# Kernel tuning notes

Hardware: AMD Instinct MI355X
Metric: run time of the kernel (lower is better)

Reference implementation:

```python
import jax, jax.numpy as jnp
import numpy as np

NUM_HEADS = 12
D_MODEL = 768


def setup_inputs() -> dict:
    key = jax.random.key(0)
    k1, k2, k3 = jax.random.split(key, 3)
    proj_std = (2.0 / (D_MODEL + D_MODEL)) ** 0.5
    in_features = jax.random.normal(k1, (4, 2048, D_MODEL), dtype=jnp.float32)
    qkv_proj_weight = (jax.random.truncated_normal(k2, -3.0, 3.0, (3, D_MODEL, D_MODEL), dtype=jnp.float32) * proj_std)
    o_proj_weight = (jax.random.truncated_normal(k3, -3.0, 3.0, (D_MODEL, D_MODEL), dtype=jnp.float32) * proj_std)
    return {"in_features": in_features, "qkv_proj_weight": qkv_proj_weight, "o_proj_weight": o_proj_weight}


def _attention(x, qkv_w, o_w):
    b, s, d = x.shape
    h = NUM_HEADS
    dk = d // h
    # Q,K,V: x @ W^T where W is (out, in) = ((h dk), d_model)
    qkv = jnp.einsum('bsd,tod->tbso', x, qkv_w)  # (3, b, s, d)
    qkv = qkv.reshape(3, b, s, h, dk).transpose(0, 1, 3, 2, 4)  # (3, b, h, s, dk)
    Q, K, V = qkv[0], qkv[1], qkv[2]
    scores = jnp.einsum('bhqd,bhkd->bhqk', Q, K) / jnp.sqrt(jnp.float32(dk))
    causal = jnp.tril(jnp.ones((s, s), dtype=bool))
    scores = jnp.where(causal, scores, -jnp.inf)
    A = jax.nn.softmax(scores, axis=-1)
    O = jnp.einsum('bhqk,bhkd->bhqd', A, V)  # (b, h, s, dk)
    O = O.transpose(0, 2, 1, 3).reshape(b, s, d)
    return jnp.einsum('bsd,od->bso', O, o_w)


def reference(in_features, qkv_proj_weight, o_proj_weight):
    return _attention(in_features, qkv_proj_weight, o_proj_weight)
```

## Files before the change

### kernel.cpp

```cpp
#include <hip/hip_runtime.h>
#include <hip/hip_bf16.h>
#include <stdint.h>

#define SEQ 2048
#define NB 4
#define NH 12
#define DMODEL 768
#define DK 64
#define NTOK (NB*SEQ)
#define QSCALE 0.18033688011f

#define N_X4   (NTOK*DMODEL/4)
#define N_WQ4  (3*DMODEL*DMODEL/4)
#define N_WO4  (DMODEL*DMODEL/4)

typedef __bf16 bf16_t;
typedef __attribute__((ext_vector_type(4))) bf16_t bf16x4;
typedef __attribute__((ext_vector_type(8))) bf16_t bf16x8;
typedef __attribute__((ext_vector_type(4))) float f32x4;

typedef __attribute__((address_space(3))) uint32_t lds_u32_t;
typedef const __attribute__((address_space(1))) uint32_t glb_u32_t;

__device__ inline void load_lds16(const void* g, void* l) {
    __builtin_amdgcn_global_load_lds((glb_u32_t*)g, (lds_u32_t*)l, 16, 0, 0);
}

__global__ void cvt_all(const float* __restrict__ x, const float* __restrict__ wq,
                        const float* __restrict__ wo, bf16_t* __restrict__ dst) {
    int i = blockIdx.x * blockDim.x + threadIdx.x;
    const float* src; int off;
    if (i < N_X4)              { src = x;  off = i; }
    else if (i < N_X4 + N_WQ4) { src = wq; off = i - N_X4; }
    else                       { src = wo; off = i - (N_X4 + N_WQ4); }
    float4 v = ((const float4*)src)[off];
    bf16x4 o;
    o[0] = (bf16_t)v.x; o[1] = (bf16_t)v.y; o[2] = (bf16_t)v.z; o[3] = (bf16_t)v.w;
    ((bf16x4*)dst)[i] = o;
}

#define QSTAGE(AS, BS, KB) do { \
    _Pragma("unroll") \
    for (int j = 0; j < 5; j++) { \
        int c = tid + j*256; \
        if (c < 512) { \
            int row = c >> 2, cb = (c & 3) * 8; \
            load_lds16(Ap_ + (size_t)(mt*128 + row)*DMODEL + (KB) + cb, AS + c*8); \
        } else { \
            int c2 = c - 512; \
            int row = c2 >> 2, cb = (c2 & 3) * 8; \
            load_lds16(Bp_ + (size_t)(nt*192 + row)*DMODEL + (KB) + cb, BS + c2*8); \
        } \
    } \
} while (0)

#define QCOMPUTE(AS, BS) do { \
    bf16x8 af[4]; \
    _Pragma("unroll") \
    for (int f = 0; f < 4; f++) \
        af[f] = *(const bf16x8*)(AS + (wy*64 + f*16 + lr)*32 + lq*8); \
    _Pragma("unroll") \
    for (int fn = 0; fn < 6; fn++) { \
        bf16x8 bfr = *(const bf16x8*)(BS + (wx*96 + fn*16 + lr)*32 + lq*8); \
        _Pragma("unroll") \
        for (int fm = 0; fm < 4; fm++) \
            acc[fm][fn] = __builtin_amdgcn_mfma_f32_16x16x32_bf16(af[fm], bfr, acc[fm][fn], 0, 0, 0); \
    } \
} while (0)

__global__ __launch_bounds__(256, 3) void gemm_qkv(
    const bf16_t* __restrict__ Ap_, const bf16_t* __restrict__ Bp_,
    bf16_t* __restrict__ Qo, bf16_t* __restrict__ Ko, bf16_t* __restrict__ VTo)
{
    __shared__ bf16_t As0[128*32];
    __shared__ bf16_t Bs0[192*32];
    __shared__ bf16_t As1[128*32];
    __shared__ bf16_t Bs1[192*32];
    const int mt = blockIdx.x, nt = blockIdx.y;
    const int tid = threadIdx.x;
    const int w = tid >> 6, lane = tid & 63;
    const int wx = w & 1, wy = w >> 1;
    const int lr = lane & 15, lq = lane >> 4;

    f32x4 acc[4][6] = {};
    QSTAGE(As0, Bs0, 0);
    for (int kb = 0; kb < DMODEL; kb += 64) {
        __syncthreads();
        QSTAGE(As1, Bs1, kb + 32);
        QCOMPUTE(As0, Bs0);
        __syncthreads();
        if (kb + 64 < DMODEL) QSTAGE(As0, Bs0, kb + 64);
        QCOMPUTE(As1, Bs1);
    }

    const int t = nt >> 2;
    const int ob = (nt & 3) * 192 + wx * 96;
    if (t == 2) {
        #pragma unroll
        for (int fm = 0; fm < 4; fm++)
            #pragma unroll
            for (int fn = 0; fn < 6; fn++) {
                int m0 = mt*128 + wy*64 + fm*16 + lq*4;
                int o = ob + fn*16 + lr;
                int b = m0 >> 11, s0 = m0 & 2047;
                int h = o >> 6, dk = o & 63;
                bf16x4 v4;
                #pragma unroll
                for (int r = 0; r < 4; r++) v4[r] = (bf16_t)acc[fm][fn][r];
                *(bf16x4*)(VTo + (size_t)((b*NH + h)*DK + dk)*SEQ + s0) = v4;
            }
    } else {
        #pragma unroll
        for (int fm = 0; fm < 4; fm++)
            #pragma unroll
            for (int fn = 0; fn < 6; fn++)
                #pragma unroll
                for (int r = 0; r < 4; r++) {
                    int m = mt*128 + wy*64 + fm*16 + lq*4 + r;
                    int o = ob + fn*16 + lr;
                    int b = m >> 11, s = m & 2047;
                    int h = o >> 6, dk = o & 63;
                    float v = acc[fm][fn][r];
                    if (t == 0) Qo[(size_t)((b*NH + h)*SEQ + s)*DK + dk] = (bf16_t)(v * QSCALE);
                    else        Ko[(size_t)((b*NH + h)*SEQ + s)*DK + dk] = (bf16_t)v;
                }
    }
}

#define OSTAGE(AS, BS, KB) do { \
    _Pragma("unroll") \
    for (int j = 0; j < 3; j++) { \
        int c = tid + j*256; \
        if (c < 512) { \
            int row = c >> 2, cb = (c & 3) * 8; \
            load_lds16(Ap_ + (size_t)(mt*128 + row)*DMODEL + (KB) + cb, AS + c*8); \
        } else { \
            int c2 = c - 512; \
            int row = c2 >> 2, cb = (c2 & 3) * 8; \
            load_lds16(Bp_ + (size_t)(nt*64 + row)*DMODEL + (KB) + cb, BS + c2*8); \
        } \
    } \
} while (0)

#define OCOMPUTE(AS, BS) do { \
    bf16x8 af[4], bfr[2]; \
    _Pragma("unroll") \
    for (int f = 0; f < 4; f++) \
        af[f]  = *(const bf16x8*)(AS + (wy*64 + f*16 + lr)*32 + lq*8); \
    _Pragma("unroll") \
    for (int f = 0; f < 2; f++) \
        bfr[f] = *(const bf16x8*)(BS + (wx*32 + f*16 + lr)*32 + lq*8); \
    _Pragma("unroll") \
    for (int fm = 0; fm < 4; fm++) \
        _Pragma("unroll") \
        for (int fn = 0; fn < 2; fn++) \
            acc[fm][fn] = __builtin_amdgcn_mfma_f32_16x16x32_bf16(af[fm], bfr[fn], acc[fm][fn], 0, 0, 0); \
} while (0)

__global__ __launch_bounds__(256, 4) void gemm_oproj(
    const bf16_t* __restrict__ Ap_, const bf16_t* __restrict__ Bp_, float* __restrict__ out)
{
    __shared__ bf16_t As0[128*32];
    __shared__ bf16_t Bs0[64*32];
    __shared__ bf16_t As1[128*32];
    __shared__ bf16_t Bs1[64*32];
    const int mt = blockIdx.x, nt = blockIdx.y;
    const int tid = threadIdx.x;
    const int w = tid >> 6, lane = tid & 63;
    const int wx = w & 1, wy = w >> 1;
    const int lr = lane & 15, lq = lane >> 4;

    f32x4 acc[4][2] = {};
    OSTAGE(As0, Bs0, 0);
    for (int kb = 0; kb < DMODEL; kb += 64) {
        __syncthreads();
        OSTAGE(As1, Bs1, kb + 32);
        OCOMPUTE(As0, Bs0);
        __syncthreads();
        if (kb + 64 < DMODEL) OSTAGE(As0, Bs0, kb + 64);
        OCOMPUTE(As1, Bs1);
    }

    #pragma unroll
    for (int fm = 0; fm < 4; fm++)
        #pragma unroll
        for (int fn = 0; fn < 2; fn++)
            #pragma unroll
            for (int r = 0; r < 4; r++) {
                int m = mt*128 + wy*64 + fm*16 + lq*4 + r;
                int n = nt*64 + wx*32 + fn*16 + lr;
                out[(size_t)m*DMODEL + n] = acc[fm][fn][r];
            }
}

#define ASTAGE(KS, VS, KB) do { \
    _Pragma("unroll") \
    for (int j = 0; j < 2; j++) { \
        int rr = w*16 + j*8 + srow; \
        int kperm = (j*8 + srow)*4 + w;   \
        load_lds16(Kp + (size_t)((KB) + kperm)*DK + g*8,  &KS[w*1024 + j*512 + lane*8]); \
        load_lds16(Vp + (size_t)rr*SEQ + (KB) + g*8,   &VS[w*1024 + j*512 + lane*8]); \
    } \
} while (0)

#define STRIP(A0, A1, ACC, AL, MASKED) do { \
    f32x4 sc[4]; \
    _Pragma("unroll") \
    for (int ct = 0; ct < 4; ct++) { \
        f32x4 s = {}; \
        s = __builtin_amdgcn_mfma_f32_16x16x32_bf16(A0, bk[ct][0], s, 0, 0, 0); \
        s = __builtin_amdgcn_mfma_f32_16x16x32_bf16(A1, bk[ct][1], s, 0, 0, 0); \
        sc[ct] = s; \
    } \
    _Pragma("unroll") \
    for (int r = 0; r < 4; r++) { \
        bf16x4 p4; \
        _Pragma("unroll") \
        for (int ct = 0; ct < 4; ct++) { \
            float p = __builtin_amdgcn_exp2f(sc[ct][r]); \
            if (MASKED) { \
                int kl = lr*4 + ct, ql = w*16 + lq*4 + r; \
                p = (kl <= ql) ? p : 0.0f; \
            } \
            p4[ct] = (bf16_t)p; \
        } \
        *(bf16x4*)(Pw + ((((lr>>3)*512 + (lq*4 + r + 16*((lr>>1)&3))*8 + (lr&1)*4)) ^ (((lr>>1)&3) << 4))) = p4; \
    } \
    { \
        bf16x8 ap0 = *(const bf16x8*)(Pw + ((lane ^ (lq<<1))*8)); \
        bf16x8 ap1 = *(const bf16x8*)(Pw + 512 + ((lane ^ (lq<<1))*8)); \
        _Pragma("unroll") \
        for (int c = 0; c < 4; c++) { \
            ACC[c] = __builtin_amdgcn_mfma_f32_16x16x32_bf16(ap0, bv[c][0], ACC[c], 0, 0, 0); \
            ACC[c] = __builtin_amdgcn_mfma_f32_16x16x32_bf16(ap1, bv[c][1], ACC[c], 0, 0, 0); \
        } \
        AL = __builtin_amdgcn_mfma_f32_16x16x32_bf16(ap0, ones, AL, 0, 0, 0); \
        AL = __builtin_amdgcn_mfma_f32_16x16x32_bf16(ap1, ones, AL, 0, 0, 0); \
    } \
} while (0)

#define AITER(KSC, VSC, KSN, VSN, T) do { \
    __syncthreads(); \
    if ((T) + 1 < nIter) ASTAGE(KSN, VSN, ((T)+1)*64); \
    bf16x8 bk[4][2], bv[4][2]; \
    const int sw = lr & 7; \
    _Pragma("unroll") \
    for (int ct = 0; ct < 4; ct++) { \
        int row = ct*16 + lr; \
        bk[ct][0] = *(const bf16x8*)(&KSC[row*64 + ((lq    ) ^ sw)*8]); \
        bk[ct][1] = *(const bf16x8*)(&KSC[row*64 + ((lq + 4) ^ sw)*8]); \
        bv[ct][0] = *(const bf16x8*)(&VSC[row*64 + ((lq    ) ^ sw)*8]); \
        bv[ct][1] = *(const bf16x8*)(&VSC[row*64 + ((lq + 4) ^ sw)*8]); \
    } \
    if ((T) <= qtA) { \
        if ((T) == qtA) { STRIP(aqA0, aqA1, accA, alA, true); } \
        else            { STRIP(aqA0, aqA1, accA, alA, false); } \
    } \
    if ((T) == nIter - 1) { STRIP(aqB0, aqB1, accB, alB, true); } \
    else                  { STRIP(aqB0, aqB1, accB, alB, false); } \
} while (0)

__global__ __launch_bounds__(256, 3) void attn(
    const bf16_t* __restrict__ Q, const bf16_t* __restrict__ K,
    const bf16_t* __restrict__ VT, bf16_t* __restrict__ O)
{
    __shared__ bf16_t Ks0[64*64];
    __shared__ bf16_t Vs0[64*64];
    __shared__ bf16_t Ks1[64*64];
    __shared__ bf16_t Vs1[64*64];
    __shared__ bf16_t P[4][1024];

    const int bh  = blockIdx.x;
    const int qtA = blockIdx.y;
    const int qtB = 31 - qtA;
    const int w = threadIdx.x >> 6, lane = threadIdx.x & 63;
    const int lr = lane & 15, lq = lane >> 4;
    const int qsA = qtA*64 + w*16;
    const int qsB = qtB*64 + w*16;
    const int srow = lane >> 3;
    const int g    = (lane & 7) ^ srow;

    const bf16_t* Qp = Q  + (size_t)bh*SEQ*DK;
    const bf16_t* Kp = K  + (size_t)bh*SEQ*DK;
    const bf16_t* Vp = VT + (size_t)bh*DK*SEQ;
    bf16_t* Pw = &P[w][0];

    const bf16x8 aqA0 = *(const bf16x8*)(Qp + (size_t)(qsA+lr)*DK + lq*8);
    const bf16x8 aqA1 = *(const bf16x8*)(Qp + (size_t)(qsA+lr)*DK + 32 + lq*8);
    const bf16x8 aqB0 = *(const bf16x8*)(Qp + (size_t)(qsB+lr)*DK + lq*8);
    const bf16x8 aqB1 = *(const bf16x8*)(Qp + (size_t)(qsB+lr)*DK + 32 + lq*8);

    bf16x8 ones;
    #pragma unroll
    for (int i = 0; i < 8; i++) ones[i] = (bf16_t)1.0f;

    f32x4 accA[4] = {}, accB[4] = {};
    f32x4 alA = {}, alB = {};

    const int nIter = 32 - qtA;

    ASTAGE(Ks0, Vs0, 0);
    int t = 0;
    while (true) {
        AITER(Ks0, Vs0, Ks1, Vs1, t); t++;
        if (t >= nIter) break;
        AITER(Ks1, Vs1, Ks0, Vs0, t); t++;
        if (t >= nIter) break;
    }

    const int b = bh / NH, h = bh % NH;
    #pragma unroll
    for (int r = 0; r < 4; r++) {
        float rlA = 1.0f / alA[r];
        float rlB = 1.0f / alB[r];
        int qa = qsA + lq*4 + r;
        int qb = qsB + lq*4 + r;
        bf16_t* opA = O + (size_t)(b*SEQ + qa)*DMODEL + h*DK;
        bf16_t* opB = O + (size_t)(b*SEQ + qb)*DMODEL + h*DK;
        #pragma unroll
        for (int c = 0; c < 4; c++) {
            opA[c*16 + lr] = (bf16_t)(accA[c][r] * rlA);
            opB[c*16 + lr] = (bf16_t)(accB[c][r] * rlB);
        }
    }
}

extern "C" void kernel_launch(void* const* d_in, const int* in_sizes, int n_in,
                              void* d_out, int out_size, void* d_ws, size_t ws_size,
                              hipStream_t stream) {
    const float* x    = (const float*)d_in[0];
    const float* wqkv = (const float*)d_in[1];
    const float* wo   = (const float*)d_in[2];
    float* out = (float*)d_out;

    char* ws = (char*)d_ws;
    const size_t SZ_X   = (size_t)NTOK*DMODEL*2;
    const size_t SZ_WQ  = (size_t)3*DMODEL*DMODEL*2;
    const size_t SZ_WO  = (size_t)DMODEL*DMODEL*2;
    const size_t SZ_HD  = (size_t)NB*NH*SEQ*DK*2;
    bf16_t* xb    = (bf16_t*)(ws);
    bf16_t* wqkvb = (bf16_t*)(ws + SZ_X);
    bf16_t* wob   = (bf16_t*)(ws + SZ_X + SZ_WQ);
    bf16_t* Qb    = (bf16_t*)(ws + SZ_X + SZ_WQ + SZ_WO);
    bf16_t* Kb    = (bf16_t*)(ws + SZ_X + SZ_WQ + SZ_WO + SZ_HD);
    bf16_t* VTb   = (bf16_t*)(ws + SZ_X + SZ_WQ + SZ_WO + 2*SZ_HD);
    bf16_t* Ob    = (bf16_t*)(ws + SZ_X + SZ_WQ + SZ_WO + 3*SZ_HD);

    cvt_all<<<(N_X4 + N_WQ4 + N_WO4) / 256, 256, 0, stream>>>(x, wqkv, wo, xb);

    gemm_qkv<<<dim3(NTOK/128, 3*DMODEL/192), 256, 0, stream>>>(xb, wqkvb, Qb, Kb, VTb);
    attn<<<dim3(NB*NH, 16), 256, 0, stream>>>(Qb, Kb, VTb, Ob);
    gemm_oproj<<<dim3(NTOK/128, DMODEL/64), 256, 0, stream>>>(Ob, wob, out);
}
```

Before: 178.9 us.

## Replace paired causal q-tile blocks with one q-tile per block, longest first

Measured after the change: 216.1 us. 1.21x slower.

```diff
diff --git a/kernel.cpp b/kernel.cpp
--- a/kernel.cpp
+++ b/kernel.cpp
@@ -252,15 +252,11 @@
         bv[ct][0] = *(const bf16x8*)(&VSC[row*64 + ((lq    ) ^ sw)*8]); \
         bv[ct][1] = *(const bf16x8*)(&VSC[row*64 + ((lq + 4) ^ sw)*8]); \
     } \
-    if ((T) <= qtA) { \
-        if ((T) == qtA) { STRIP(aqA0, aqA1, accA, alA, true); } \
-        else            { STRIP(aqA0, aqA1, accA, alA, false); } \
-    } \
-    if ((T) == nIter - 1) { STRIP(aqB0, aqB1, accB, alB, true); } \
-    else                  { STRIP(aqB0, aqB1, accB, alB, false); } \
-} while (0)
-
-__global__ __launch_bounds__(256, 3) void attn(
+    if ((T) == nIter - 1) { STRIP(aq0, aq1, acc, al, true); } \
+    else                  { STRIP(aq0, aq1, acc, al, false); } \
+} while (0)
+
+__global__ __launch_bounds__(256, 4) void attn(
     const bf16_t* __restrict__ Q, const bf16_t* __restrict__ K,
     const bf16_t* __restrict__ VT, bf16_t* __restrict__ O)
 {
@@ -271,12 +267,10 @@
     __shared__ bf16_t P[4][1024];
 
     const int bh  = blockIdx.x;
-    const int qtA = blockIdx.y;
-    const int qtB = 31 - qtA;
+    const int qt  = 31 - blockIdx.y;
     const int w = threadIdx.x >> 6, lane = threadIdx.x & 63;
     const int lr = lane & 15, lq = lane >> 4;
-    const int qsA = qtA*64 + w*16;
-    const int qsB = qtB*64 + w*16;
+    const int qs = qt*64 + w*16;
     const int srow = lane >> 3;
     const int g    = (lane & 7) ^ srow;
 
@@ -285,19 +279,17 @@
     const bf16_t* Vp = VT + (size_t)bh*DK*SEQ;
     bf16_t* Pw = &P[w][0];
 
-    const bf16x8 aqA0 = *(const bf16x8*)(Qp + (size_t)(qsA+lr)*DK + lq*8);
-    const bf16x8 aqA1 = *(const bf16x8*)(Qp + (size_t)(qsA+lr)*DK + 32 + lq*8);
-    const bf16x8 aqB0 = *(const bf16x8*)(Qp + (size_t)(qsB+lr)*DK + lq*8);
-    const bf16x8 aqB1 = *(const bf16x8*)(Qp + (size_t)(qsB+lr)*DK + 32 + lq*8);
+    const bf16x8 aq0 = *(const bf16x8*)(Qp + (size_t)(qs+lr)*DK + lq*8);
+    const bf16x8 aq1 = *(const bf16x8*)(Qp + (size_t)(qs+lr)*DK + 32 + lq*8);
 
     bf16x8 ones;
     #pragma unroll
     for (int i = 0; i < 8; i++) ones[i] = (bf16_t)1.0f;
 
-    f32x4 accA[4] = {}, accB[4] = {};
-    f32x4 alA = {}, alB = {};
-
-    const int nIter = 32 - qtA;
+    f32x4 acc[4] = {};
+    f32x4 al = {};
+
+    const int nIter = qt + 1;
 
     ASTAGE(Ks0, Vs0, 0);
     int t = 0;
@@ -311,17 +303,12 @@
     const int b = bh / NH, h = bh % NH;
     #pragma unroll
     for (int r = 0; r < 4; r++) {
-        float rlA = 1.0f / alA[r];
-        float rlB = 1.0f / alB[r];
-        int qa = qsA + lq*4 + r;
-        int qb = qsB + lq*4 + r;
-        bf16_t* opA = O + (size_t)(b*SEQ + qa)*DMODEL + h*DK;
-        bf16_t* opB = O + (size_t)(b*SEQ + qb)*DMODEL + h*DK;
+        float rl = 1.0f / al[r];
+        int q = qs + lq*4 + r;
+        bf16_t* op = O + (size_t)(b*SEQ + q)*DMODEL + h*DK;
         #pragma unroll
-        for (int c = 0; c < 4; c++) {
-            opA[c*16 + lr] = (bf16_t)(accA[c][r] * rlA);
-            opB[c*16 + lr] = (bf16_t)(accB[c][r] * rlB);
-        }
+        for (int c = 0; c < 4; c++)
+            op[c*16 + lr] = (bf16_t)(acc[c][r] * rl);
     }
 }
 
@@ -349,6 +336,6 @@
     cvt_all<<<(N_X4 + N_WQ4 + N_WO4) / 256, 256, 0, stream>>>(x, wqkv, wo, xb);
 
     gemm_qkv<<<dim3(NTOK/128, 3*DMODEL/192), 256, 0, stream>>>(xb, wqkvb, Qb, Kb, VTb);
-    attn<<<dim3(NB*NH, 16), 256, 0, stream>>>(Qb, Kb, VTb, Ob);
+    attn<<<dim3(NB*NH, 32), 256, 0, stream>>>(Qb, Kb, VTb, Ob);
     gemm_oproj<<<dim3(NTOK/128, DMODEL/64), 256, 0, stream>>>(Ob, wob, out);
 }
```

## Keep softmax probabilities in registers via transposed score MFMA, drop LDS round-trip

Applied to the files above, without the earlier changes.

After: 176.3 us. No clear change (-1.4%).

```diff
diff --git a/kernel.cpp b/kernel.cpp
--- a/kernel.cpp
+++ b/kernel.cpp
@@ -197,45 +197,42 @@
     _Pragma("unroll") \
     for (int j = 0; j < 2; j++) { \
         int rr = w*16 + j*8 + srow; \
-        int kperm = (j*8 + srow)*4 + w;   \
+        int kperm = (w>>1)*32 + (j*2 + (srow>>2))*8 + (w&1)*4 + (srow&3);   \
         load_lds16(Kp + (size_t)((KB) + kperm)*DK + g*8,  &KS[w*1024 + j*512 + lane*8]); \
         load_lds16(Vp + (size_t)rr*SEQ + (KB) + g*8,   &VS[w*1024 + j*512 + lane*8]); \
     } \
 } while (0)
 
-#define STRIP(A0, A1, ACC, AL, MASKED) do { \
+#define STRIP(A0, A1, ACC, DL, MASKED) do { \
     f32x4 sc[4]; \
     _Pragma("unroll") \
     for (int ct = 0; ct < 4; ct++) { \
         f32x4 s = {}; \
-        s = __builtin_amdgcn_mfma_f32_16x16x32_bf16(A0, bk[ct][0], s, 0, 0, 0); \
-        s = __builtin_amdgcn_mfma_f32_16x16x32_bf16(A1, bk[ct][1], s, 0, 0, 0); \
+        s = __builtin_amdgcn_mfma_f32_16x16x32_bf16(bk[ct][0], A0, s, 0, 0, 0); \
+        s = __builtin_amdgcn_mfma_f32_16x16x32_bf16(bk[ct][1], A1, s, 0, 0, 0); \
         sc[ct] = s; \
     } \
-    _Pragma("unroll") \
-    for (int r = 0; r < 4; r++) { \
-        bf16x4 p4; \
+    bf16x8 ap0, ap1; \
+    _Pragma("unroll") \
+    for (int ct = 0; ct < 4; ct++) { \
         _Pragma("unroll") \
-        for (int ct = 0; ct < 4; ct++) { \
+        for (int r = 0; r < 4; r++) { \
             float p = __builtin_amdgcn_exp2f(sc[ct][r]); \
             if (MASKED) { \
-                int kl = lr*4 + ct, ql = w*16 + lq*4 + r; \
+                int kl = (ct>>1)*32 + lq*8 + (ct&1)*4 + r; \
+                int ql = w*16 + lr; \
                 p = (kl <= ql) ? p : 0.0f; \
             } \
-            p4[ct] = (bf16_t)p; \
+            bf16_t pb = (bf16_t)p; \
+            DL += (float)pb; \
+            if (ct < 2) ap0[(ct&1)*4 + r] = pb; \
+            else        ap1[(ct&1)*4 + r] = pb; \
         } \
-        *(bf16x4*)(Pw + ((((lr>>3)*512 + (lq*4 + r + 16*((lr>>1)&3))*8 + (lr&1)*4)) ^ (((lr>>1)&3) << 4))) = p4; \
-    } \
-    { \
-        bf16x8 ap0 = *(const bf16x8*)(Pw + ((lane ^ (lq<<1))*8)); \
-        bf16x8 ap1 = *(const bf16x8*)(Pw + 512 + ((lane ^ (lq<<1))*8)); \
-        _Pragma("unroll") \
-        for (int c = 0; c < 4; c++) { \
-            ACC[c] = __builtin_amdgcn_mfma_f32_16x16x32_bf16(ap0, bv[c][0], ACC[c], 0, 0, 0); \
-            ACC[c] = __builtin_amdgcn_mfma_f32_16x16x32_bf16(ap1, bv[c][1], ACC[c], 0, 0, 0); \
-        } \
-        AL = __builtin_amdgcn_mfma_f32_16x16x32_bf16(ap0, ones, AL, 0, 0, 0); \
-        AL = __builtin_amdgcn_mfma_f32_16x16x32_bf16(ap1, ones, AL, 0, 0, 0); \
+    } \
+    _Pragma("unroll") \
+    for (int c = 0; c < 4; c++) { \
+        ACC[c] = __builtin_amdgcn_mfma_f32_16x16x32_bf16(ap0, bv[c][0], ACC[c], 0, 0, 0); \
+        ACC[c] = __builtin_amdgcn_mfma_f32_16x16x32_bf16(ap1, bv[c][1], ACC[c], 0, 0, 0); \
     } \
 } while (0)
 
@@ -253,11 +250,11 @@
         bv[ct][1] = *(const bf16x8*)(&VSC[row*64 + ((lq + 4) ^ sw)*8]); \
     } \
     if ((T) <= qtA) { \
-        if ((T) == qtA) { STRIP(aqA0, aqA1, accA, alA, true); } \
-        else            { STRIP(aqA0, aqA1, accA, alA, false); } \
-    } \
-    if ((T) == nIter - 1) { STRIP(aqB0, aqB1, accB, alB, true); } \
-    else                  { STRIP(aqB0, aqB1, accB, alB, false); } \
+        if ((T) == qtA) { STRIP(aqA0, aqA1, accA, dlA, true); } \
+        else            { STRIP(aqA0, aqA1, accA, dlA, false); } \
+    } \
+    if ((T) == nIter - 1) { STRIP(aqB0, aqB1, accB, dlB, true); } \
+    else                  { STRIP(aqB0, aqB1, accB, dlB, false); } \
 } while (0)
 
 __global__ __launch_bounds__(256, 3) void attn(
@@ -268,7 +265,6 @@
     __shared__ bf16_t Vs0[64*64];
     __shared__ bf16_t Ks1[64*64];
     __shared__ bf16_t Vs1[64*64];
-    __shared__ bf16_t P[4][1024];
 
     const int bh  = blockIdx.x;
     const int qtA = blockIdx.y;
@@ -283,19 +279,14 @@
     const bf16_t* Qp = Q  + (size_t)bh*SEQ*DK;
     const bf16_t* Kp = K  + (size_t)bh*SEQ*DK;
     const bf16_t* Vp = VT + (size_t)bh*DK*SEQ;
-    bf16_t* Pw = &P[w][0];
 
     const bf16x8 aqA0 = *(const bf16x8*)(Qp + (size_t)(qsA+lr)*DK + lq*8);
     const bf16x8 aqA1 = *(const bf16x8*)(Qp + (size_t)(qsA+lr)*DK + 32 + lq*8);
     const bf16x8 aqB0 = *(const bf16x8*)(Qp + (size_t)(qsB+lr)*DK + lq*8);
     const bf16x8 aqB1 = *(const bf16x8*)(Qp + (size_t)(qsB+lr)*DK + 32 + lq*8);
 
-    bf16x8 ones;
-    #pragma unroll
-    for (int i = 0; i < 8; i++) ones[i] = (bf16_t)1.0f;
-
     f32x4 accA[4] = {}, accB[4] = {};
-    f32x4 alA = {}, alB = {};
+    float dlA = 0.0f, dlB = 0.0f;
 
     const int nIter = 32 - qtA;
 
@@ -308,11 +299,14 @@
         if (t >= nIter) break;
     }
 
+    dlA += __shfl_xor(dlA, 16, 64); dlA += __shfl_xor(dlA, 32, 64);
+    dlB += __shfl_xor(dlB, 16, 64); dlB += __shfl_xor(dlB, 32, 64);
+
     const int b = bh / NH, h = bh % NH;
     #pragma unroll
     for (int r = 0; r < 4; r++) {
-        float rlA = 1.0f / alA[r];
-        float rlB = 1.0f / alB[r];
+        float rlA = 1.0f / __shfl(dlA, lq*4 + r, 64);
+        float rlB = 1.0f / __shfl(dlB, lq*4 + r, 64);
         int qa = qsA + lq*4 + r;
         int qb = qsB + lq*4 + r;
         bf16_t* opA = O + (size_t)(b*SEQ + qa)*DMODEL + h*DK;
```

## Keep attention P in registers via transposed QK^T; swizzle GEMM LDS tiles

Applied to the files above, without the earlier changes.

Result: faster. 174.3 us (-2.5%).

```diff
diff --git a/kernel.cpp b/kernel.cpp
--- a/kernel.cpp
+++ b/kernel.cpp
@@ -44,11 +44,11 @@
     for (int j = 0; j < 5; j++) { \
         int c = tid + j*256; \
         if (c < 512) { \
-            int row = c >> 2, cb = (c & 3) * 8; \
+            int row = c >> 2, cb = ((c & 3) ^ ((c >> 3) & 3)) * 8; \
             load_lds16(Ap_ + (size_t)(mt*128 + row)*DMODEL + (KB) + cb, AS + c*8); \
         } else { \
             int c2 = c - 512; \
-            int row = c2 >> 2, cb = (c2 & 3) * 8; \
+            int row = c2 >> 2, cb = ((c2 & 3) ^ ((c2 >> 3) & 3)) * 8; \
             load_lds16(Bp_ + (size_t)(nt*192 + row)*DMODEL + (KB) + cb, BS + c2*8); \
         } \
     } \
@@ -58,10 +58,10 @@
     bf16x8 af[4]; \
     _Pragma("unroll") \
     for (int f = 0; f < 4; f++) \
-        af[f] = *(const bf16x8*)(AS + (wy*64 + f*16 + lr)*32 + lq*8); \
+        af[f] = *(const bf16x8*)(AS + (wy*32 + f*8 + lh)*64 + xr); \
     _Pragma("unroll") \
     for (int fn = 0; fn < 6; fn++) { \
-        bf16x8 bfr = *(const bf16x8*)(BS + (wx*96 + fn*16 + lr)*32 + lq*8); \
+        bf16x8 bfr = *(const bf16x8*)(BS + (wx*48 + fn*8 + lh)*64 + xr); \
         _Pragma("unroll") \
         for (int fm = 0; fm < 4; fm++) \
             acc[fm][fn] = __builtin_amdgcn_mfma_f32_16x16x32_bf16(af[fm], bfr, acc[fm][fn], 0, 0, 0); \
@@ -81,6 +81,8 @@
     const int w = tid >> 6, lane = tid & 63;
     const int wx = w & 1, wy = w >> 1;
     const int lr = lane & 15, lq = lane >> 4;
+    const int lh = lr >> 1;
+    const int xr = (lr & 1)*32 + ((lq ^ (lh & 3)) * 8);
 
     f32x4 acc[4][6] = {};
     QSTAGE(As0, Bs0, 0);
@@ -132,11 +134,11 @@
     for (int j = 0; j < 3; j++) { \
         int c = tid + j*256; \
         if (c < 512) { \
-            int row = c >> 2, cb = (c & 3) * 8; \
+            int row = c >> 2, cb = ((c & 3) ^ ((c >> 3) & 3)) * 8; \
             load_lds16(Ap_ + (size_t)(mt*128 + row)*DMODEL + (KB) + cb, AS + c*8); \
         } else { \
             int c2 = c - 512; \
-            int row = c2 >> 2, cb = (c2 & 3) * 8; \
+            int row = c2 >> 2, cb = ((c2 & 3) ^ ((c2 >> 3) & 3)) * 8; \
             load_lds16(Bp_ + (size_t)(nt*64 + row)*DMODEL + (KB) + cb, BS + c2*8); \
         } \
     } \
@@ -146,10 +148,10 @@
     bf16x8 af[4], bfr[2]; \
     _Pragma("unroll") \
     for (int f = 0; f < 4; f++) \
-        af[f]  = *(const bf16x8*)(AS + (wy*64 + f*16 + lr)*32 + lq*8); \
+        af[f]  = *(const bf16x8*)(AS + (wy*32 + f*8 + lh)*64 + xr); \
     _Pragma("unroll") \
     for (int f = 0; f < 2; f++) \
-        bfr[f] = *(const bf16x8*)(BS + (wx*32 + f*16 + lr)*32 + lq*8); \
+        bfr[f] = *(const bf16x8*)(BS + (wx*16 + f*8 + lh)*64 + xr); \
     _Pragma("unroll") \
     for (int fm = 0; fm < 4; fm++) \
         _Pragma("unroll") \
@@ -169,6 +171,8 @@
     const int w = tid >> 6, lane = tid & 63;
     const int wx = w & 1, wy = w >> 1;
     const int lr = lane & 15, lq = lane >> 4;
+    const int lh = lr >> 1;
+    const int xr = (lr & 1)*32 + ((lq ^ (lh & 3)) * 8);
 
     f32x4 acc[4][2] = {};
     OSTAGE(As0, Bs0, 0);
@@ -197,7 +201,7 @@
     _Pragma("unroll") \
     for (int j = 0; j < 2; j++) { \
         int rr = w*16 + j*8 + srow; \
-        int kperm = (j*8 + srow)*4 + w;   \
+        int kperm = (w>>1)*32 + (j*2 + (srow>>2))*8 + (w&1)*4 + (srow&3);   \
         load_lds16(Kp + (size_t)((KB) + kperm)*DK + g*8,  &KS[w*1024 + j*512 + lane*8]); \
         load_lds16(Vp + (size_t)rr*SEQ + (KB) + g*8,   &VS[w*1024 + j*512 + lane*8]); \
     } \
@@ -208,35 +212,33 @@
     _Pragma("unroll") \
     for (int ct = 0; ct < 4; ct++) { \
         f32x4 s = {}; \
-        s = __builtin_amdgcn_mfma_f32_16x16x32_bf16(A0, bk[ct][0], s, 0, 0, 0); \
-        s = __builtin_amdgcn_mfma_f32_16x16x32_bf16(A1, bk[ct][1], s, 0, 0, 0); \
+        s = __builtin_amdgcn_mfma_f32_16x16x32_bf16(bk[ct][0], A0, s, 0, 0, 0); \
+        s = __builtin_amdgcn_mfma_f32_16x16x32_bf16(bk[ct][1], A1, s, 0, 0, 0); \
         sc[ct] = s; \
     } \
-    _Pragma("unroll") \
-    for (int r = 0; r < 4; r++) { \
-        bf16x4 p4; \
+    bf16x8 ap0, ap1; \
+    _Pragma("unroll") \
+    for (int ct = 0; ct < 4; ct++) { \
         _Pragma("unroll") \
-        for (int ct = 0; ct < 4; ct++) { \
+        for (int r = 0; r < 4; r++) { \
             float p = __builtin_amdgcn_exp2f(sc[ct][r]); \
             if (MASKED) { \
-                int kl = lr*4 + ct, ql = w*16 + lq*4 + r; \
+                int kl = (ct>>1)*32 + lq*8 + (ct&1)*4 + r; \
+                int ql = w*16 + lr; \
                 p = (kl <= ql) ? p : 0.0f; \
             } \
-            p4[ct] = (bf16_t)p; \
+            bf16_t pb = (bf16_t)p; \
+            if (ct < 2) ap0[(ct&1)*4 + r] = pb; \
+            else        ap1[(ct&1)*4 + r] = pb; \
         } \
-        *(bf16x4*)(Pw + ((((lr>>3)*512 + (lq*4 + r + 16*((lr>>1)&3))*8 + (lr&1)*4)) ^ (((lr>>1)&3) << 4))) = p4; \
-    } \
-    { \
-        bf16x8 ap0 = *(const bf16x8*)(Pw + ((lane ^ (lq<<1))*8)); \
-        bf16x8 ap1 = *(const bf16x8*)(Pw + 512 + ((lane ^ (lq<<1))*8)); \
-        _Pragma("unroll") \
-        for (int c = 0; c < 4; c++) { \
-            ACC[c] = __builtin_amdgcn_mfma_f32_16x16x32_bf16(ap0, bv[c][0], ACC[c], 0, 0, 0); \
-            ACC[c] = __builtin_amdgcn_mfma_f32_16x16x32_bf16(ap1, bv[c][1], ACC[c], 0, 0, 0); \
-        } \
-        AL = __builtin_amdgcn_mfma_f32_16x16x32_bf16(ap0, ones, AL, 0, 0, 0); \
-        AL = __builtin_amdgcn_mfma_f32_16x16x32_bf16(ap1, ones, AL, 0, 0, 0); \
-    } \
+    } \
+    _Pragma("unroll") \
+    for (int c = 0; c < 4; c++) { \
+        ACC[c] = __builtin_amdgcn_mfma_f32_16x16x32_bf16(ap0, bv[c][0], ACC[c], 0, 0, 0); \
+        ACC[c] = __builtin_amdgcn_mfma_f32_16x16x32_bf16(ap1, bv[c][1], ACC[c], 0, 0, 0); \
+    } \
+    AL = __builtin_amdgcn_mfma_f32_16x16x32_bf16(ap0, ones, AL, 0, 0, 0); \
+    AL = __builtin_amdgcn_mfma_f32_16x16x32_bf16(ap1, ones, AL, 0, 0, 0); \
 } while (0)
 
 #define AITER(KSC, VSC, KSN, VSN, T) do { \
@@ -268,7 +270,6 @@
     __shared__ bf16_t Vs0[64*64];
     __shared__ bf16_t Ks1[64*64];
     __shared__ bf16_t Vs1[64*64];
-    __shared__ bf16_t P[4][1024];
 
     const int bh  = blockIdx.x;
     const int qtA = blockIdx.y;
@@ -283,7 +284,6 @@
     const bf16_t* Qp = Q  + (size_t)bh*SEQ*DK;
     const bf16_t* Kp = K  + (size_t)bh*SEQ*DK;
     const bf16_t* Vp = VT + (size_t)bh*DK*SEQ;
-    bf16_t* Pw = &P[w][0];
 
     const bf16x8 aqA0 = *(const bf16x8*)(Qp + (size_t)(qsA+lr)*DK + lq*8);
     const bf16x8 aqA1 = *(const bf16x8*)(Qp + (size_t)(qsA+lr)*DK + 32 + lq*8);
```
